# Kernel optimization log

Hardware: AMD Instinct MI355X
Metric: run time of the kernel (lower is better)

## Reference

```python
import jax, jax.numpy as jnp
import numpy as np

B, A, I, D = 4, 32, 512, 256


def setup_inputs() -> dict:
    key = jax.random.key(0)
    k0, k1, kw1, kw2, ka1, ka2 = jax.random.split(key, 6)
    return {
        "i0": jax.random.normal(k0, (B, A, I, D), dtype=jnp.float32),
        "i1": jax.random.normal(k1, (B, A, I, D), dtype=jnp.float32),
        "W1": jax.random.normal(kw1, (D, D), dtype=jnp.float32) * 0.02,
        "W2": jax.random.normal(kw2, (D, D), dtype=jnp.float32) * 0.02,
        "attn1": jax.random.normal(ka1, (D, D), dtype=jnp.float32) * 0.02,
        "attn2": jax.random.normal(ka2, (D, D), dtype=jnp.float32) * 0.02,
    }


def reference(i0, i1, W1, W2, attn1, attn2):
    # Bilinear gating scores: sum_j sum_k x1[...,j] * A[j,k] * x0[...,k] -> [b,a,i]
    g0 = jax.nn.sigmoid(jnp.einsum('baij,jk,baik->bai', i1, attn1, i0))
    g1 = jax.nn.sigmoid(jnp.einsum('baij,jk,baik->bai', i0, attn2, i1))
    # Gated residual: x += x * gate
    r0 = i0 + i0 * g0[..., None]
    r1 = i1 + i1 * g1[..., None]
    # Dual projection sum
    return jnp.einsum('baij,jk->baik', r0, W1) + jnp.einsum('baij,jk->baik', r1, W2)
```

## Files before the change

kernel.cpp:

```cpp
#include <hip/hip_runtime.h>

#define D256 256
#define TOTROWS 65536
#define BM 64
#define LDW 264
#define NBLK (TOTROWS / BM)
#define NT 512

typedef unsigned short u16;
typedef unsigned int u32;
typedef __attribute__((ext_vector_type(8))) short bf16x8;
typedef __attribute__((ext_vector_type(16))) float f32x16;

__device__ __forceinline__ float b2f(u16 u) {
  union { u32 i; float f; } v; v.i = ((u32)u) << 16; return v.f;
}
__device__ __forceinline__ u16 f2b(float f) {
  union { float f; u32 i; } v; v.f = f;
  return (u16)((v.i + 0x7fffu + ((v.i >> 16) & 1u)) >> 16);
}
__device__ __forceinline__ u32 f2b2(float lo, float hi) {
  u32 r;
  asm("v_cvt_pk_bf16_f32 %0, %1, %2" : "=v"(r) : "v"(lo), "v"(hi));
  return r;
}

__global__ void build_wfrag(const float* __restrict__ a1,
                            const float* __restrict__ a2,
                            const float* __restrict__ W1,
                            const float* __restrict__ W2,
                            u16* __restrict__ Wf) {
  const int m = blockIdx.y;
  const int idx = blockIdx.x * 256 + threadIdx.x;
  int col, c;
  const float* src;
  if (m < 2) { col = idx >> 5; c = idx & 31; src = m ? a2 : a1; }
  else       { col = idx & 255; c = idx >> 8; src = (m == 3) ? W2 : W1; }
  const int kk0 = c * 8;
  const int p = col >> 5, l31 = col & 31, lhh = c & 1, k = c >> 1;
  const int ln = lhh * 32 + l31;
  u16* dst = Wf + m * 65536 + ((p * 16 + k) * 64 + ln) * 8;
  u16 v[8];
  if (m < 2) {
#pragma unroll
    for (int j = 0; j < 8; j++) v[j] = f2b(src[col * 256 + kk0 + j]);
  } else {
#pragma unroll
    for (int j = 0; j < 8; j++) v[j] = f2b(src[(kk0 + j) * 256 + col]);
  }
  ushort4 lo, hi;
  lo.x = v[0]; lo.y = v[1]; lo.z = v[2]; lo.w = v[3];
  hi.x = v[4]; hi.y = v[5]; hi.z = v[6]; hi.w = v[7];
  ((ushort4*)dst)[0] = lo;
  ((ushort4*)dst)[1] = hi;
}

__global__ __launch_bounds__(NT, 4)
void fused(const float* __restrict__ X0g, const float* __restrict__ X1g,
           const u16* __restrict__ Wf, float* __restrict__ outg) {
  __shared__ u16 lX0[BM][LDW];
  __shared__ u16 lX1[BM][LDW];
  __shared__ float sp0[BM], sp1[BM], sc0[BM], sc1[BM];

  const int t = threadIdx.x;
  const int row0 = blockIdx.x * BM;

  if (t < BM) { sp0[t] = 0.f; }
  else if (t < 2 * BM) { sp1[t - BM] = 0.f; }

  {
    const float4* g0 = (const float4*)(X0g + (size_t)row0 * D256);
    const float4* g1 = (const float4*)(X1g + (size_t)row0 * D256);
    uint2* s0 = (uint2*)&lX0[0][0];
    uint2* s1 = (uint2*)&lX1[0][0];
#pragma unroll 4
    for (int i = 0; i < 8; i++) {
      const int e = i * NT + t;
      const int row = e >> 6;
      const int col = e & 63;
      float4 a = g0[e];
      float4 b = g1[e];
      uint2 pa, pb;
      pa.x = f2b2(a.x, a.y); pa.y = f2b2(a.z, a.w);
      pb.x = f2b2(b.x, b.y); pb.y = f2b2(b.z, b.w);
      s0[row * 66 + col] = pa;
      s1[row * 66 + col] = pb;
    }
  }
  __syncthreads();

  const int ln  = t & 63;
  const int wv  = t >> 6;
  const int l31 = ln & 31;
  const int lh  = ln >> 5;
  const int cb  = wv * 32;

  const u16* wA1 = Wf + 0 * 65536 + (wv * 16) * 512 + ln * 8;
  const u16* wA2 = Wf + 1 * 65536 + (wv * 16) * 512 + ln * 8;
  const u16* wW1 = Wf + 2 * 65536 + (wv * 16) * 512 + ln * 8;
  const u16* wW2 = Wf + 3 * 65536 + (wv * 16) * 512 + ln * 8;

  {
    f32x16 G0a, G0b, G1a, G1b;
#pragma unroll
    for (int i = 0; i < 16; i++) { G0a[i] = 0.f; G0b[i] = 0.f;
                                   G1a[i] = 0.f; G1b[i] = 0.f; }

#pragma unroll 2
    for (int k = 0; k < 16; k++) {
      bf16x8 w1 = *(const bf16x8*)(wA1 + k * 512);
      bf16x8 w2 = *(const bf16x8*)(wA2 + k * 512);
      bf16x8 a0a = *(const bf16x8*)(&lX0[l31][k * 16 + lh * 8]);
      bf16x8 a0b = *(const bf16x8*)(&lX0[32 + l31][k * 16 + lh * 8]);
      bf16x8 a1a = *(const bf16x8*)(&lX1[l31][k * 16 + lh * 8]);
      bf16x8 a1b = *(const bf16x8*)(&lX1[32 + l31][k * 16 + lh * 8]);
      G0a = __builtin_amdgcn_mfma_f32_32x32x16_bf16(w1, a0a, G0a, 0, 0, 0);
      G0b = __builtin_amdgcn_mfma_f32_32x32x16_bf16(w1, a0b, G0b, 0, 0, 0);
      G1a = __builtin_amdgcn_mfma_f32_32x32x16_bf16(w2, a1a, G1a, 0, 0, 0);
      G1b = __builtin_amdgcn_mfma_f32_32x32x16_bf16(w2, a1b, G1b, 0, 0, 0);
    }

#pragma unroll
    for (int tt = 0; tt < 2; tt++) {
      const u16* xr1 = &lX1[tt * 32 + l31][cb + 4 * lh];
      const u16* xr0 = &lX0[tt * 32 + l31][cb + 4 * lh];
      const f32x16& Gt0 = tt ? G0b : G0a;
      const f32x16& Gt1 = tt ? G1b : G1a;
      float v0 = 0.f, v1 = 0.f;
#pragma unroll
      for (int g = 0; g < 4; g++) {
        ushort4 a = *(const ushort4*)(xr1 + 8 * g);
        ushort4 b = *(const ushort4*)(xr0 + 8 * g);
        v0 += Gt0[g * 4 + 0] * b2f(a.x) + Gt0[g * 4 + 1] * b2f(a.y) +
              Gt0[g * 4 + 2] * b2f(a.z) + Gt0[g * 4 + 3] * b2f(a.w);
        v1 += Gt1[g * 4 + 0] * b2f(b.x) + Gt1[g * 4 + 1] * b2f(b.y) +
              Gt1[g * 4 + 2] * b2f(b.z) + Gt1[g * 4 + 3] * b2f(b.w);
      }
      v0 += __shfl_xor(v0, 32, 64);
      v1 += __shfl_xor(v1, 32, 64);
      if (lh == 0) {
        atomicAdd(&sp0[tt * 32 + l31], v0);
        atomicAdd(&sp1[tt * 32 + l31], v1);
      }
    }
  }
  __syncthreads();

  if (t < BM) {
    sc0[t] = 1.f + 1.f / (1.f + __expf(-sp0[t]));
  } else if (t < 2 * BM) {
    sc1[t - BM] = 1.f + 1.f / (1.f + __expf(-sp1[t - BM]));
  }

  {
    f32x16 P0a, P0b, P1a, P1b;
#pragma unroll
    for (int i = 0; i < 16; i++) { P0a[i] = 0.f; P0b[i] = 0.f;
                                   P1a[i] = 0.f; P1b[i] = 0.f; }

#pragma unroll 2
    for (int k = 0; k < 16; k++) {
      bf16x8 w1 = *(const bf16x8*)(wW1 + k * 512);
      bf16x8 w2 = *(const bf16x8*)(wW2 + k * 512);
      bf16x8 a0a = *(const bf16x8*)(&lX0[l31][k * 16 + lh * 8]);
      bf16x8 a0b = *(const bf16x8*)(&lX0[32 + l31][k * 16 + lh * 8]);
      bf16x8 a1a = *(const bf16x8*)(&lX1[l31][k * 16 + lh * 8]);
      bf16x8 a1b = *(const bf16x8*)(&lX1[32 + l31][k * 16 + lh * 8]);
      P0a = __builtin_amdgcn_mfma_f32_32x32x16_bf16(a0a, w1, P0a, 0, 0, 0);
      P0b = __builtin_amdgcn_mfma_f32_32x32x16_bf16(a0b, w1, P0b, 0, 0, 0);
      P1a = __builtin_amdgcn_mfma_f32_32x32x16_bf16(a1a, w2, P1a, 0, 0, 0);
      P1b = __builtin_amdgcn_mfma_f32_32x32x16_bf16(a1b, w2, P1b, 0, 0, 0);
    }

    __syncthreads();

    float* opb = outg + (size_t)row0 * 256 + cb;
#pragma unroll
    for (int q = 0; q < 4; q++) {
      float s0a[4], s1a[4], s0b[4], s1b[4];
      *(float4*)s0a = *(const float4*)&sc0[8 * q + 4 * lh];
      *(float4*)s1a = *(const float4*)&sc1[8 * q + 4 * lh];
      *(float4*)s0b = *(const float4*)&sc0[32 + 8 * q + 4 * lh];
      *(float4*)s1b = *(const float4*)&sc1[32 + 8 * q + 4 * lh];
#pragma unroll
      for (int j = 0; j < 4; j++) {
        const int r = q * 4 + j;
        const int row = j + 8 * q + 4 * lh;
        __builtin_nontemporal_store(s0a[j] * P0a[r] + s1a[j] * P1a[r],
                                    &opb[row * 256 + l31]);
        __builtin_nontemporal_store(s0b[j] * P0b[r] + s1b[j] * P1b[r],
                                    &opb[(32 + row) * 256 + l31]);
      }
    }
  }
}

extern "C" void kernel_launch(void* const* d_in, const int* in_sizes, int n_in,
                              void* d_out, int out_size, void* d_ws, size_t ws_size,
                              hipStream_t stream) {
  const float* i0 = (const float*)d_in[0];
  const float* i1 = (const float*)d_in[1];
  const float* W1 = (const float*)d_in[2];
  const float* W2 = (const float*)d_in[3];
  const float* a1 = (const float*)d_in[4];
  const float* a2 = (const float*)d_in[5];
  u16* Wf = (u16*)d_ws;

  build_wfrag<<<dim3(32, 4), 256, 0, stream>>>(a1, a2, W1, W2, Wf);
  fused<<<NBLK, NT, 0, stream>>>(i0, i1, Wf, (float*)d_out);
}
```

Measured before the change: 203.7 us.

## Retile waves to 32 rows by 64 columns and pad LDS row stride

```diff
diff --git a/kernel.cpp b/kernel.cpp
--- a/kernel.cpp
+++ b/kernel.cpp
@@ -3,7 +3,7 @@
 #define D256 256
 #define TOTROWS 65536
 #define BM 64
-#define LDW 264
+#define LDW 268
 #define NBLK (TOTROWS / BM)
 #define NT 512
 
@@ -83,8 +83,8 @@
       uint2 pa, pb;
       pa.x = f2b2(a.x, a.y); pa.y = f2b2(a.z, a.w);
       pb.x = f2b2(b.x, b.y); pb.y = f2b2(b.z, b.w);
-      s0[row * 66 + col] = pa;
-      s1[row * 66 + col] = pb;
+      s0[row * 67 + col] = pa;
+      s1[row * 67 + col] = pb;
     }
   }
   __syncthreads();
@@ -93,54 +93,67 @@
   const int wv  = t >> 6;
   const int l31 = ln & 31;
   const int lh  = ln >> 5;
-  const int cb  = wv * 32;
-
-  const u16* wA1 = Wf + 0 * 65536 + (wv * 16) * 512 + ln * 8;
-  const u16* wA2 = Wf + 1 * 65536 + (wv * 16) * 512 + ln * 8;
-  const u16* wW1 = Wf + 2 * 65536 + (wv * 16) * 512 + ln * 8;
-  const u16* wW2 = Wf + 3 * 65536 + (wv * 16) * 512 + ln * 8;
+  const int rt  = wv >> 2;
+  const int rb  = rt * 32;
+  const int pq  = wv & 3;
+  const int cb0 = (2 * pq) * 32;
+  const int cb1 = (2 * pq + 1) * 32;
+
+  const u16* w_[4][2];
+#pragma unroll
+  for (int m = 0; m < 4; m++) {
+#pragma unroll
+    for (int pp = 0; pp < 2; pp++) {
+      w_[m][pp] = Wf + m * 65536 + ((2 * pq + pp) * 16) * 512 + ln * 8;
+    }
+  }
 
   {
-    f32x16 G0a, G0b, G1a, G1b;
-#pragma unroll
-    for (int i = 0; i < 16; i++) { G0a[i] = 0.f; G0b[i] = 0.f;
-                                   G1a[i] = 0.f; G1b[i] = 0.f; }
+    f32x16 G00, G01, G10, G11;
+#pragma unroll
+    for (int i = 0; i < 16; i++) { G00[i] = 0.f; G01[i] = 0.f;
+                                   G10[i] = 0.f; G11[i] = 0.f; }
 
 #pragma unroll 2
     for (int k = 0; k < 16; k++) {
-      bf16x8 w1 = *(const bf16x8*)(wA1 + k * 512);
-      bf16x8 w2 = *(const bf16x8*)(wA2 + k * 512);
-      bf16x8 a0a = *(const bf16x8*)(&lX0[l31][k * 16 + lh * 8]);
-      bf16x8 a0b = *(const bf16x8*)(&lX0[32 + l31][k * 16 + lh * 8]);
-      bf16x8 a1a = *(const bf16x8*)(&lX1[l31][k * 16 + lh * 8]);
-      bf16x8 a1b = *(const bf16x8*)(&lX1[32 + l31][k * 16 + lh * 8]);
-      G0a = __builtin_amdgcn_mfma_f32_32x32x16_bf16(w1, a0a, G0a, 0, 0, 0);
-      G0b = __builtin_amdgcn_mfma_f32_32x32x16_bf16(w1, a0b, G0b, 0, 0, 0);
-      G1a = __builtin_amdgcn_mfma_f32_32x32x16_bf16(w2, a1a, G1a, 0, 0, 0);
-      G1b = __builtin_amdgcn_mfma_f32_32x32x16_bf16(w2, a1b, G1b, 0, 0, 0);
-    }
-
-#pragma unroll
-    for (int tt = 0; tt < 2; tt++) {
-      const u16* xr1 = &lX1[tt * 32 + l31][cb + 4 * lh];
-      const u16* xr0 = &lX0[tt * 32 + l31][cb + 4 * lh];
-      const f32x16& Gt0 = tt ? G0b : G0a;
-      const f32x16& Gt1 = tt ? G1b : G1a;
+      bf16x8 a0 = *(const bf16x8*)(&lX0[rb + l31][k * 16 + lh * 8]);
+      bf16x8 a1 = *(const bf16x8*)(&lX1[rb + l31][k * 16 + lh * 8]);
+      bf16x8 w10 = *(const bf16x8*)(w_[0][0] + k * 512);
+      bf16x8 w11 = *(const bf16x8*)(w_[0][1] + k * 512);
+      bf16x8 w20 = *(const bf16x8*)(w_[1][0] + k * 512);
+      bf16x8 w21 = *(const bf16x8*)(w_[1][1] + k * 512);
+      G00 = __builtin_amdgcn_mfma_f32_32x32x16_bf16(w10, a0, G00, 0, 0, 0);
+      G01 = __builtin_amdgcn_mfma_f32_32x32x16_bf16(w11, a0, G01, 0, 0, 0);
+      G10 = __builtin_amdgcn_mfma_f32_32x32x16_bf16(w20, a1, G10, 0, 0, 0);
+      G11 = __builtin_amdgcn_mfma_f32_32x32x16_bf16(w21, a1, G11, 0, 0, 0);
+    }
+
+    {
+      const u16* xr1a = &lX1[rb + l31][cb0 + 4 * lh];
+      const u16* xr1b = &lX1[rb + l31][cb1 + 4 * lh];
+      const u16* xr0a = &lX0[rb + l31][cb0 + 4 * lh];
+      const u16* xr0b = &lX0[rb + l31][cb1 + 4 * lh];
       float v0 = 0.f, v1 = 0.f;
 #pragma unroll
       for (int g = 0; g < 4; g++) {
-        ushort4 a = *(const ushort4*)(xr1 + 8 * g);
-        ushort4 b = *(const ushort4*)(xr0 + 8 * g);
-        v0 += Gt0[g * 4 + 0] * b2f(a.x) + Gt0[g * 4 + 1] * b2f(a.y) +
-              Gt0[g * 4 + 2] * b2f(a.z) + Gt0[g * 4 + 3] * b2f(a.w);
-        v1 += Gt1[g * 4 + 0] * b2f(b.x) + Gt1[g * 4 + 1] * b2f(b.y) +
-              Gt1[g * 4 + 2] * b2f(b.z) + Gt1[g * 4 + 3] * b2f(b.w);
+        ushort4 a = *(const ushort4*)(xr1a + 8 * g);
+        ushort4 b = *(const ushort4*)(xr1b + 8 * g);
+        ushort4 c = *(const ushort4*)(xr0a + 8 * g);
+        ushort4 d = *(const ushort4*)(xr0b + 8 * g);
+        v0 += G00[g * 4 + 0] * b2f(a.x) + G00[g * 4 + 1] * b2f(a.y) +
+              G00[g * 4 + 2] * b2f(a.z) + G00[g * 4 + 3] * b2f(a.w);
+        v0 += G01[g * 4 + 0] * b2f(b.x) + G01[g * 4 + 1] * b2f(b.y) +
+              G01[g * 4 + 2] * b2f(b.z) + G01[g * 4 + 3] * b2f(b.w);
+        v1 += G10[g * 4 + 0] * b2f(c.x) + G10[g * 4 + 1] * b2f(c.y) +
+              G10[g * 4 + 2] * b2f(c.z) + G10[g * 4 + 3] * b2f(c.w);
+        v1 += G11[g * 4 + 0] * b2f(d.x) + G11[g * 4 + 1] * b2f(d.y) +
+              G11[g * 4 + 2] * b2f(d.z) + G11[g * 4 + 3] * b2f(d.w);
       }
       v0 += __shfl_xor(v0, 32, 64);
       v1 += __shfl_xor(v1, 32, 64);
       if (lh == 0) {
-        atomicAdd(&sp0[tt * 32 + l31], v0);
-        atomicAdd(&sp1[tt * 32 + l31], v1);
+        atomicAdd(&sp0[rb + l31], v0);
+        atomicAdd(&sp1[rb + l31], v1);
       }
     }
   }
@@ -153,43 +166,44 @@
   }
 
   {
-    f32x16 P0a, P0b, P1a, P1b;
-#pragma unroll
-    for (int i = 0; i < 16; i++) { P0a[i] = 0.f; P0b[i] = 0.f;
-                                   P1a[i] = 0.f; P1b[i] = 0.f; }
+    f32x16 P00, P01, P10, P11;
+#pragma unroll
+    for (int i = 0; i < 16; i++) { P00[i] = 0.f; P01[i] = 0.f;
+                                   P10[i] = 0.f; P11[i] = 0.f; }
 
 #pragma unroll 2
     for (int k = 0; k < 16; k++) {
-      bf16x8 w1 = *(const bf16x8*)(wW1 + k * 512);
-      bf16x8 w2 = *(const bf16x8*)(wW2 + k * 512);
-      bf16x8 a0a = *(const bf16x8*)(&lX0[l31][k * 16 + lh * 8]);
-      bf16x8 a0b = *(const bf16x8*)(&lX0[32 + l31][k * 16 + lh * 8]);
-      bf16x8 a1a = *(const bf16x8*)(&lX1[l31][k * 16 + lh * 8]);
-      bf16x8 a1b = *(const bf16x8*)(&lX1[32 + l31][k * 16 + lh * 8]);
-      P0a = __builtin_amdgcn_mfma_f32_32x32x16_bf16(a0a, w1, P0a, 0, 0, 0);
-      P0b = __builtin_amdgcn_mfma_f32_32x32x16_bf16(a0b, w1, P0b, 0, 0, 0);
-      P1a = __builtin_amdgcn_mfma_f32_32x32x16_bf16(a1a, w2, P1a, 0, 0, 0);
-      P1b = __builtin_amdgcn_mfma_f32_32x32x16_bf16(a1b, w2, P1b, 0, 0, 0);
+      bf16x8 a0 = *(const bf16x8*)(&lX0[rb + l31][k * 16 + lh * 8]);
+      bf16x8 a1 = *(const bf16x8*)(&lX1[rb + l31][k * 16 + lh * 8]);
+      bf16x8 u10 = *(const bf16x8*)(w_[2][0] + k * 512);
+      bf16x8 u11 = *(const bf16x8*)(w_[2][1] + k * 512);
+      bf16x8 u20 = *(const bf16x8*)(w_[3][0] + k * 512);
+      bf16x8 u21 = *(const bf16x8*)(w_[3][1] + k * 512);
+      P00 = __builtin_amdgcn_mfma_f32_32x32x16_bf16(a0, u10, P00, 0, 0, 0);
+      P01 = __builtin_amdgcn_mfma_f32_32x32x16_bf16(a0, u11, P01, 0, 0, 0);
+      P10 = __builtin_amdgcn_mfma_f32_32x32x16_bf16(a1, u20, P10, 0, 0, 0);
+      P11 = __builtin_amdgcn_mfma_f32_32x32x16_bf16(a1, u21, P11, 0, 0, 0);
     }
 
     __syncthreads();
 
-    float* opb = outg + (size_t)row0 * 256 + cb;
-#pragma unroll
-    for (int q = 0; q < 4; q++) {
-      float s0a[4], s1a[4], s0b[4], s1b[4];
-      *(float4*)s0a = *(const float4*)&sc0[8 * q + 4 * lh];
-      *(float4*)s1a = *(const float4*)&sc1[8 * q + 4 * lh];
-      *(float4*)s0b = *(const float4*)&sc0[32 + 8 * q + 4 * lh];
-      *(float4*)s1b = *(const float4*)&sc1[32 + 8 * q + 4 * lh];
-#pragma unroll
-      for (int j = 0; j < 4; j++) {
-        const int r = q * 4 + j;
-        const int row = j + 8 * q + 4 * lh;
-        __builtin_nontemporal_store(s0a[j] * P0a[r] + s1a[j] * P1a[r],
-                                    &opb[row * 256 + l31]);
-        __builtin_nontemporal_store(s0b[j] * P0b[r] + s1b[j] * P1b[r],
-                                    &opb[(32 + row) * 256 + l31]);
+#pragma unroll
+    for (int pp = 0; pp < 2; pp++) {
+      float* opb = outg + (size_t)(row0 + rb) * D256 + (pp ? cb1 : cb0);
+#pragma unroll
+      for (int q = 0; q < 4; q++) {
+        float s0a[4], s1a[4];
+        *(float4*)s0a = *(const float4*)&sc0[rb + 8 * q + 4 * lh];
+        *(float4*)s1a = *(const float4*)&sc1[rb + 8 * q + 4 * lh];
+#pragma unroll
+        for (int j = 0; j < 4; j++) {
+          const int r = q * 4 + j;
+          const int row = j + 8 * q + 4 * lh;
+          const float p0 = pp ? P01[r] : P00[r];
+          const float p1 = pp ? P11[r] : P10[r];
+          __builtin_nontemporal_store(s0a[j] * p0 + s1a[j] * p1,
+                                      &opb[row * D256 + l31]);
+        }
       }
     }
   }
```

Result: slower. 208.0 us (+2.1%).
